# Kernel optimization log

Measured on AMD Instinct MI355X. Metric: run time of the kernel, lower is better.

The kernel has to match this reference:

```python
import jax, jax.numpy as jnp
import numpy as np
from jax import lax

B, D, H, W = 1, 16, 128, 128
CIN, NPTS = 16, 100000
NEG = np.float32(-1e30)  # stands in for -inf at unoccupied voxels in max pooling


def _conv(x, wk):
    # Minkowski stride-1 conv at occupied sites == dense zero-padded conv masked to occupancy
    return lax.conv_general_dilated(x, wk, (1, 1, 1), 'SAME',
                                    dimension_numbers=('NCDHW', 'OIDHW', 'NCDHW'))


def _crelu(x, wk, occ):
    return jnp.where(occ, jax.nn.relu(_conv(x, wk)), 0.0)


def _mpool(x, occ, spatial):
    # Minkowski max pool: max over occupied voxels in the kernel window; output coords are
    # the stride-floored input coords (z halved). spatial=True -> kernel (3,3,3) else (3,1,1).
    xm = jnp.where(occ, x, NEG)
    win = (1, 1, 3, 3, 3) if spatial else (1, 1, 3, 1, 1)
    pad = [(0, 0), (0, 0), (1, 1), (1, 1), (1, 1)] if spatial else [(0, 0), (0, 0), (1, 1), (0, 0), (0, 0)]
    y = lax.reduce_window(xm, NEG, lax.max, win, (1, 1, 2, 1, 1), pad)
    occ2 = occ[:, :, 0::2] | occ[:, :, 1::2]
    return jnp.where(occ2, y, 0.0), occ2


def _forward(voxel_features, coors, ws, batch_size):
    b, d, h, w = coors[:, 0], coors[:, 1], coors[:, 2], coors[:, 3]
    cin = voxel_features.shape[1]
    grid = jnp.zeros((batch_size, D, H, W, cin), voxel_features.dtype).at[b, d, h, w].set(voxel_features)
    x = jnp.transpose(grid, (0, 4, 1, 2, 3))  # (B, C, D, H, W)
    occ = jnp.zeros((batch_size, 1, D, H, W), bool).at[b, 0, d, h, w].set(True)

    x = _crelu(x, ws[0], occ)
    x = _crelu(x, ws[1], occ)
    x, occ = _mpool(x, occ, True)
    for wk in ws[2:5]:
        x = _crelu(x, wk, occ)
    x, occ = _mpool(x, occ, True)
    for wk in ws[5:8]:
        x = _crelu(x, wk, occ)
    x, occ = _mpool(x, occ, False)  # kernel (3,1,1)
    n, c, dd, hh, ww = x.shape  # (B, 64, 2, H, W)
    return x.reshape(n, c * dd, hh, ww)


def setup_inputs():
    key = jax.random.key(0)
    ks = jax.random.split(key, 9)
    rng = np.random.default_rng(0)
    lin = rng.permutation(D * H * W)[:NPTS].astype(np.int64)  # unique occupied voxels
    d = (lin // (H * W)).astype(np.int32)
    h = ((lin // W) % H).astype(np.int32)
    w = (lin % W).astype(np.int32)
    coors = jnp.asarray(np.stack([np.zeros(NPTS, np.int32), d, h, w], axis=1))
    vf = jax.random.normal(ks[0], (NPTS, CIN), jnp.float32)

    def cw(k, o, i):
        return jax.random.normal(k, (o, i, 3, 3, 3), jnp.float32) * np.float32(1.0 / np.sqrt(i * 27))

    chans = [(32, CIN), (64, 32)] + [(64, 64)] * 6
    ws = {f"w{j + 1}": cw(ks[j + 1], o, i) for j, (o, i) in enumerate(chans)}
    return dict(voxel_features=vf, coors=coors, batch_size=B, **ws)


def reference(voxel_features, coors, batch_size, w1, w2, w3, w4, w5, w6, w7, w8):
    return _forward(voxel_features, coors, (w1, w2, w3, w4, w5, w6, w7, w8), batch_size)
```

## Files before the change

### kernel.cpp

```cpp
#include <hip/hip_runtime.h>
#include <stdint.h>

#define DEV __device__ __forceinline__

typedef float f32x4 __attribute__((ext_vector_type(4)));
typedef short s16x8 __attribute__((ext_vector_type(8)));
typedef unsigned int u32x4 __attribute__((ext_vector_type(4)));
typedef unsigned int u32x2 __attribute__((ext_vector_type(2)));

static constexpr int HM = 128, WM = 128;
static constexpr int HP = 130, WP = 130;

DEV unsigned short f2bf(float f) {
  unsigned int u = __float_as_uint(f);
  return (unsigned short)((u + 0x7fffu + ((u >> 16) & 1u)) >> 16);
}
DEV float bf2f(unsigned short s) { return __uint_as_float(((unsigned int)s) << 16); }

DEV void gll16(const void* g, void* l) {
  __builtin_amdgcn_global_load_lds((const unsigned int*)g, (unsigned int*)l, 16, 0, 0);
}
DEV void waitvmc(int n) {
  if (n == 0)      asm volatile("s_waitcnt vmcnt(0)" ::: "memory");
  else if (n == 1) asm volatile("s_waitcnt vmcnt(1)" ::: "memory");
  else if (n == 2) asm volatile("s_waitcnt vmcnt(2)" ::: "memory");
  else if (n == 3) asm volatile("s_waitcnt vmcnt(3)" ::: "memory");
  else if (n == 4) asm volatile("s_waitcnt vmcnt(4)" ::: "memory");
  else if (n == 5) asm volatile("s_waitcnt vmcnt(5)" ::: "memory");
  else if (n == 7) asm volatile("s_waitcnt vmcnt(7)" ::: "memory");
  else             asm volatile("s_waitcnt vmcnt(0)" ::: "memory");
}

__global__ __launch_bounds__(256)
void scatter_k(const float* __restrict__ vf, const int* __restrict__ co,
               unsigned short* __restrict__ x,
               unsigned char* __restrict__ o0, unsigned char* __restrict__ o1,
               unsigned char* __restrict__ o2, unsigned char* __restrict__ o3,
               int npts) {
  int i = blockIdx.x * 256 + threadIdx.x;
  if (i >= npts) return;
  int d = co[i * 4 + 1], h = co[i * 4 + 2], w = co[i * 4 + 3];
  unsigned short* dst = x + (size_t)(((d + 1) * HP + (h + 1)) * WP + (w + 1)) * 32;
#pragma unroll
  for (int c = 0; c < 16; ++c) dst[c] = f2bf(vf[i * 16 + c]);
  int hw = h * WM + w;
  o0[d * (HM * WM) + hw] = 1;
  o1[(d >> 1) * (HM * WM) + hw] = 1;
  o2[(d >> 2) * (HM * WM) + hw] = 1;
  o3[(d >> 3) * (HM * WM) + hw] = 1;
}

__global__ __launch_bounds__(256)
void wcvt_all_k(const float* s0, const float* s1, const float* s2, const float* s3,
                const float* s4, const float* s5, const float* s6, const float* s7,
                unsigned short* __restrict__ dst) {
  int t = blockIdx.x * 256 + threadIdx.x;
  const int CIs[8] = {16, 32, 64, 64, 64, 64, 64, 64};
  const int CId[8] = {32, 32, 64, 64, 64, 64, 64, 64};
  const int COa[8] = {32, 64, 64, 64, 64, 64, 64, 64};
  const float* srcs[8] = {s0, s1, s2, s3, s4, s5, s6, s7};
  int start = 0;
#pragma unroll
  for (int i = 0; i < 8; ++i) {
    int sz = 27 * COa[i] * CId[i];
    if (t >= start && t < start + sz) {
      int l = t - start;
      int ci = l % CId[i];
      int r = l / CId[i];
      int cco = r % COa[i];
      int tap = r / COa[i];
      float v = (ci < CIs[i]) ? srcs[i][(cco * CIs[i] + ci) * 27 + tap] : 0.0f;
      dst[t] = f2bf(v);
    }
    start += sz;
  }
}

template <int CI, int CO, int ROWS>
__global__ __launch_bounds__(512, 4)
void conv_k(const unsigned short* __restrict__ xin, unsigned short* __restrict__ xout,
            const unsigned short* __restrict__ wt, const unsigned char* __restrict__ occ,
            int D) {
  constexpr int SLOTS = CI / 8;
  constexpr int MSK = SLOTS - 1;
  constexpr int CIB = CI / 32;
  constexpr int NM = CO / 16;
  constexpr int J = ROWS;
  constexpr int XROWS = ROWS + 2;
  constexpr int RXI = (128 * SLOTS) / 512;
  constexpr int NCW = 3 * CO * SLOTS;
  constexpr int KW = (NCW + 511) / 512;
  constexpr int NA = 2 * RXI + KW;
  constexpr int NB = RXI + KW;
  constexpr int WOFF = 3 * CO * CI;
  __shared__ __align__(16) unsigned short xs[XROWS * 130 * CI];
  __shared__ __align__(16) unsigned short wls[2 * WOFF];

  int nb = gridDim.x;
  int bid = blockIdx.x;
  int blk = (bid & 7) * (nb >> 3) + (bid >> 3);
  int tid = threadIdx.x;
  constexpr int HBLK = 128 / ROWS;
  int d = blk / HBLK, hb = blk - (blk / HBLK) * HBLK;
  int h0 = hb * ROWS;
  int lane = tid & 63, wv = tid >> 6, ln = lane & 15, lg = lane >> 4;

  auto issueX = [&](int kd, int ri) {
#pragma unroll
    for (int i = 0; i < RXI; ++i) {
      int c = i * 512 + tid;
      int vcol = 1 + c / SLOTS;
      int sl = c - (c / SLOTS) * SLOTS;
      int v = ri * 130 + vcol;
      int ss = sl ^ (v & MSK);
      const unsigned short* g =
          xin + ((size_t)((d + kd) * HP + (h0 + ri)) * WP + vcol) * CI + ss * 8;
      gll16(g, xs + (size_t)(ri * 130 + 1) * CI + (size_t)c * 8);
    }
  };
  auto issueW = [&](int kd, int kh, unsigned short* wbuf) {
#pragma unroll
    for (int i = 0; i < KW; ++i) {
      int c = i * 512 + tid;
      if (c >= NCW) c -= NCW;
      int u = c / SLOTS, sl = c - (c / SLOTS) * SLOTS;
      int kw = u / CO, cc = u - kw * CO;
      int ss = sl ^ (u & MSK);
      const unsigned short* g =
          wt + ((size_t)((kd * 3 + kh) * 3 + kw) * CO + cc) * CI + ss * 8;
      gll16(g, wbuf + (size_t)c * 8);
    }
  };

  {
    constexpr int CH8 = CO / 8;
    int hv = 2 * HP * WP + D * (2 * WP + 2 * HM);
    int tot8 = hv * CH8;
    int per = (tot8 + nb - 1) / nb;
    int base = blk * per, lim = base + per;
    if (lim > tot8) lim = tot8;
    for (int c = base + tid; c < lim; c += 512) {
      int i = c / CH8, sub = c - (c / CH8) * CH8;
      int p, hh, ww;
      if (i < 2 * HP * WP) {
        p = (i >= HP * WP) ? (D + 1) : 0;
        int rem = i - ((i >= HP * WP) ? HP * WP : 0);
        hh = rem / WP; ww = rem - hh * WP;
      } else {
        constexpr int PH = 2 * WP + 2 * HM;
        int j2 = i - 2 * HP * WP;
        p = j2 / PH + 1;
        int r2 = j2 - (p - 1) * PH;
        if (r2 < 2 * WP) { hh = (r2 >= WP) ? (HP - 1) : 0; ww = r2 % WP; }
        else { int r3 = r2 - 2 * WP; hh = 1 + (r3 & 127); ww = (r3 < HM) ? 0 : (WP - 1); }
      }
      *(u32x4*)(xout + ((size_t)(p * HP + hh) * WP + ww) * CO + sub * 8) = (u32x4)0u;
    }
  }
  issueX(0, 0);
  issueX(0, 1);
  issueW(0, 0, wls);
  for (int t = tid; t < XROWS * 2 * SLOTS; t += 512) {
    int ri = t / (2 * SLOTS);
    int r2 = t - ri * 2 * SLOTS;
    int colv = (r2 >= SLOTS) ? 129 : 0;
    int sl = r2 & MSK;
    *(u32x4*)(xs + (size_t)(ri * 130 + colv) * CI + sl * 8) = (u32x4)0u;
  }
  float on[J];
#pragma unroll
  for (int j = 0; j < J; ++j) {
    int vox = wv * (16 * J) + j * 16 + ln;
    on[j] = occ[(d * HM + (h0 + (vox >> 7))) * WM + (vox & 127)] ? 1.0f : 0.0f;
  }
  asm volatile("s_waitcnt lgkmcnt(0)" ::: "memory");

  f32x4 acc[NM][J];
#pragma unroll
  for (int m = 0; m < NM; ++m)
#pragma unroll
    for (int j = 0; j < J; ++j) acc[m][j] = (f32x4)0.0f;

#pragma unroll
  for (int s = 0; s < 9; ++s) {
    int kd = s / 3, kh = s - 3 * kd;
    unsigned short* wnext = wls + ((s + 1) & 1) * WOFF;
    if (kh == 0) {
#pragma unroll
      for (int ri = 2; ri < XROWS; ++ri) issueX(kd, ri);
      issueW(kd, 1, wnext);
    } else if (kh == 1) {
      if (kd < 2) issueX(kd + 1, 0);
      issueW(kd, 2, wnext);
    } else {
      if (kd < 2) {
        issueX(kd + 1, 1);
        issueW(kd + 1, 0, wnext);
      }
    }
    __builtin_amdgcn_sched_barrier(0);
    if (kh == 0)      waitvmc(NA);
    else if (kh == 1) waitvmc(kd < 2 ? NB : KW);
    else              waitvmc(kd < 2 ? NB : 0);
    __builtin_amdgcn_sched_barrier(0);
    __builtin_amdgcn_s_barrier();
    __builtin_amdgcn_sched_barrier(0);
    const unsigned short* wc = wls + (s & 1) * WOFF;
    __builtin_amdgcn_s_setprio(1);
#pragma unroll
    for (int kw = 0; kw < 3; ++kw) {
#pragma unroll
      for (int cb = 0; cb < CIB; ++cb) {
        int slot = cb * 4 + lg;
        s16x8 a[NM], b[J];
#pragma unroll
        for (int m = 0; m < NM; ++m) {
          int u = kw * CO + m * 16 + ln;
          a[m] = *(const s16x8*)(wc + ((size_t)u * SLOTS + (slot ^ (u & MSK))) * 8);
        }
#pragma unroll
        for (int j = 0; j < J; ++j) {
          int vox = wv * (16 * J) + j * 16 + ln;
          int v = ((vox >> 7) + kh) * 130 + (vox & 127) + kw;
          b[j] = *(const s16x8*)(xs + ((size_t)v * SLOTS + (slot ^ (v & MSK))) * 8);
        }
#pragma unroll
        for (int m = 0; m < NM; ++m)
#pragma unroll
          for (int j = 0; j < J; ++j)
            acc[m][j] = __builtin_amdgcn_mfma_f32_16x16x32_bf16(a[m], b[j], acc[m][j], 0, 0, 0);
      }
    }
    __builtin_amdgcn_s_setprio(0);
    __builtin_amdgcn_sched_barrier(0);
    if (s < 8) __builtin_amdgcn_s_barrier();
  }

#pragma unroll
  for (int j = 0; j < J; ++j) {
    int vox = wv * (16 * J) + j * 16 + ln;
    int r = vox >> 7, w2 = vox & 127;
    unsigned short* dst = xout + ((size_t)((d + 1) * HP + (h0 + r + 1)) * WP + (w2 + 1)) * CO;
#pragma unroll
    for (int m = 0; m < NM; ++m) {
      unsigned short q0 = f2bf(fmaxf(acc[m][j][0], 0.0f) * on[j]);
      unsigned short q1 = f2bf(fmaxf(acc[m][j][1], 0.0f) * on[j]);
      unsigned short q2 = f2bf(fmaxf(acc[m][j][2], 0.0f) * on[j]);
      unsigned short q3 = f2bf(fmaxf(acc[m][j][3], 0.0f) * on[j]);
      u32x2 pv;
      pv.x = (unsigned int)q0 | ((unsigned int)q1 << 16);
      pv.y = (unsigned int)q2 | ((unsigned int)q3 << 16);
      *(u32x2*)&dst[m * 16 + lg * 4] = pv;
    }
  }
}

template <int C>
__global__ __launch_bounds__(256)
void pool_sp_k(const unsigned short* __restrict__ xin, unsigned short* __restrict__ xout,
               const unsigned char* __restrict__ oc, int Dout) {
  constexpr int CH = C / 8;
  __shared__ __align__(16) unsigned short vm[WP * C];
  int row = blockIdx.x;
  int bh = row % HP, bdo = row / HP;
  int outRow = (bdo * HP + bh) * WP * C;
  int tid = threadIdx.x;
  if (bdo == 0 || bdo == Dout + 1 || bh == 0 || bh == HP - 1) {
    for (int i = tid; i < WP * C; i += 256) xout[outRow + i] = 0;
    return;
  }
  int dp = bdo - 1, h = bh - 1;

  for (int idx = tid; idx < WP * CH; idx += 256) {
    int w = idx / CH, c8 = idx - w * CH;
    float mx[8];
#pragma unroll
    for (int q = 0; q < 8; ++q) mx[q] = 0.0f;
#pragma unroll
    for (int dd = 0; dd < 3; ++dd)
#pragma unroll
      for (int hh = 0; hh < 3; ++hh) {
        const unsigned short* p =
            xin + ((size_t)((2 * dp + dd) * HP + (h + hh)) * WP + w) * C + c8 * 8;
        u32x4 v = *(const u32x4*)p;
        const unsigned short* u = (const unsigned short*)&v;
#pragma unroll
        for (int q = 0; q < 8; ++q) mx[q] = fmaxf(mx[q], bf2f(u[q]));
      }
    unsigned short o[8];
#pragma unroll
    for (int q = 0; q < 8; ++q) o[q] = f2bf(mx[q]);
    *(u32x4*)&vm[w * C + c8 * 8] = *(const u32x4*)o;
  }
  __syncthreads();

  for (int idx = tid; idx < WM * CH; idx += 256) {
    int w = idx / CH, c8 = idx - w * CH;
    float mx[8];
#pragma unroll
    for (int q = 0; q < 8; ++q) mx[q] = 0.0f;
#pragma unroll
    for (int ww = 0; ww < 3; ++ww) {
      u32x4 v = *(const u32x4*)&vm[(w + ww) * C + c8 * 8];
      const unsigned short* u = (const unsigned short*)&v;
#pragma unroll
      for (int q = 0; q < 8; ++q) mx[q] = fmaxf(mx[q], bf2f(u[q]));
    }
    bool on = oc[(dp * HM + h) * WM + w] != 0;
    unsigned short o[8];
#pragma unroll
    for (int q = 0; q < 8; ++q) o[q] = on ? f2bf(mx[q]) : (unsigned short)0;
    *(u32x4*)(xout + outRow + (w + 1) * C + c8 * 8) = *(const u32x4*)o;
  }
  for (int i = tid; i < 2 * C; i += 256) {
    int s = i / C, c = i - (i / C) * C;
    xout[outRow + (s ? (WP - 1) * C : 0) + c] = 0;
  }
}

__global__ __launch_bounds__(256)
void pool_d_k(const unsigned short* __restrict__ xin, float* __restrict__ out,
              const unsigned char* __restrict__ oc) {
  int t = blockIdx.x * 256 + threadIdx.x;
  int c8 = t & 7, w = (t >> 3) & 127, h = (t >> 10) & 127, dp = (t >> 17) & 1;
  float mx[8];
#pragma unroll
  for (int q = 0; q < 8; ++q) mx[q] = 0.0f;
#pragma unroll
  for (int dd = 0; dd < 3; ++dd) {
    const unsigned short* p =
        xin + ((size_t)((2 * dp + dd) * HP + (h + 1)) * WP + (w + 1)) * 64 + c8 * 8;
    u32x4 v = *(const u32x4*)p;
    const unsigned short* u = (const unsigned short*)&v;
#pragma unroll
    for (int q = 0; q < 8; ++q) mx[q] = fmaxf(mx[q], bf2f(u[q]));
  }
  bool on = oc[(dp * HM + h) * WM + w] != 0;
#pragma unroll
  for (int q = 0; q < 8; ++q) {
    int c = c8 * 8 + q;
    out[((c * 2 + dp) * HM + h) * WM + w] = on ? mx[q] : 0.0f;
  }
}

extern "C" void kernel_launch(void* const* d_in, const int* in_sizes, int n_in,
                              void* d_out, int out_size, void* d_ws, size_t ws_size,
                              hipStream_t stream) {
  (void)n_in; (void)out_size; (void)ws_size;
  const float* vf = (const float*)d_in[0];
  const int* co = (const int*)d_in[1];
  int npts = in_sizes[1] / 4;

  char* ws = (char*)d_ws;
  const size_t SA = (size_t)18 * 130 * 130 * 64 * 2;
  const size_t SB = (size_t)10 * 130 * 130 * 64 * 2;
  unsigned short* P = (unsigned short*)ws;
  unsigned short* Q = (unsigned short*)(ws + SA);
  unsigned short* R = P;
  unsigned char* occ0 = (unsigned char*)(ws + SA + SB);
  unsigned char* occ1 = occ0 + 16 * HM * WM;
  unsigned char* occ2 = occ1 + 8 * HM * WM;
  unsigned char* occ3 = occ2 + 4 * HM * WM;
  unsigned short* wb[8];
  {
    unsigned short* p = (unsigned short*)(occ3 + 2 * HM * WM);
    const int wsz[8] = {27 * 32 * 32, 27 * 64 * 32, 27 * 64 * 64, 27 * 64 * 64,
                        27 * 64 * 64, 27 * 64 * 64, 27 * 64 * 64, 27 * 64 * 64};
    for (int i = 0; i < 8; ++i) { wb[i] = p; p += wsz[i]; }
  }

  hipMemsetAsync(R, 0, (size_t)18 * 130 * 130 * 32 * 2, stream);
  hipMemsetAsync(occ0, 0, (size_t)(16 + 8 + 4 + 2) * HM * WM, stream);

  scatter_k<<<(npts + 255) / 256, 256, 0, stream>>>(vf, co, R, occ0, occ1, occ2, occ3, npts);

  {
    int tot = 27 * (32 * 32 + 64 * 32 + 6 * 64 * 64);
    wcvt_all_k<<<tot / 256, 256, 0, stream>>>(
        (const float*)d_in[3], (const float*)d_in[4], (const float*)d_in[5],
        (const float*)d_in[6], (const float*)d_in[7], (const float*)d_in[8],
        (const float*)d_in[9], (const float*)d_in[10], wb[0]);
  }

  conv_k<32, 32, 4><<<16 * 32, 512, 0, stream>>>(R, Q, wb[0], occ0, 16);
  conv_k<32, 64, 4><<<16 * 32, 512, 0, stream>>>(Q, P, wb[1], occ0, 16);
  pool_sp_k<64><<<10 * HP, 256, 0, stream>>>(P, Q, occ1, 8);
  conv_k<64, 64, 4><<<8 * 32, 512, 0, stream>>>(Q, P, wb[2], occ1, 8);
  conv_k<64, 64, 4><<<8 * 32, 512, 0, stream>>>(P, Q, wb[3], occ1, 8);
  conv_k<64, 64, 4><<<8 * 32, 512, 0, stream>>>(Q, P, wb[4], occ1, 8);
  pool_sp_k<64><<<6 * HP, 256, 0, stream>>>(P, Q, occ2, 4);
  conv_k<64, 64, 2><<<4 * 64, 512, 0, stream>>>(Q, P, wb[5], occ2, 4);
  conv_k<64, 64, 2><<<4 * 64, 512, 0, stream>>>(P, Q, wb[6], occ2, 4);
  conv_k<64, 64, 2><<<4 * 64, 512, 0, stream>>>(Q, P, wb[7], occ2, 4);
  pool_d_k<<<(2 * 128 * 128 * 8) / 256, 256, 0, stream>>>(P, (float*)d_out, occ3);
}
```

Measured before the change: 276.6 us.

## Tile spatial max-pool over four output rows with shared D-reduced halo

The spatial pooling kernel now processes four output H-rows per block. It first reduces over depth for six input rows and keeps them in shared memory, then does the 3x3 H/W max from LDS. Each D-reduced row is reused by three output rows instead of being reloaded from global memory. Halo zeroing is spread evenly across all blocks, and block IDs are swizzled. The grid shrinks from about 1300 blocks to 256/128, which cuts redundant global reads but lowers parallelism and uses more LDS per block.

```diff
diff --git a/kernel.cpp b/kernel.cpp
--- a/kernel.cpp
+++ b/kernel.cpp
@@ -260,61 +260,83 @@
 void pool_sp_k(const unsigned short* __restrict__ xin, unsigned short* __restrict__ xout,
                const unsigned char* __restrict__ oc, int Dout) {
   constexpr int CH = C / 8;
-  __shared__ __align__(16) unsigned short vm[WP * C];
-  int row = blockIdx.x;
-  int bh = row % HP, bdo = row / HP;
-  int outRow = (bdo * HP + bh) * WP * C;
+  __shared__ __align__(16) unsigned short dm[6 * WP * C];
+  int nb = gridDim.x;
+  int bid = blockIdx.x;
+  int blk = (bid & 7) * (nb >> 3) + (bid >> 3);
   int tid = threadIdx.x;
-  if (bdo == 0 || bdo == Dout + 1 || bh == 0 || bh == HP - 1) {
-    for (int i = tid; i < WP * C; i += 256) xout[outRow + i] = 0;
-    return;
-  }
-  int dp = bdo - 1, h = bh - 1;
-
-  for (int idx = tid; idx < WP * CH; idx += 256) {
-    int w = idx / CH, c8 = idx - w * CH;
+  int dp = blk >> 5, ht = blk & 31;
+  int h0 = ht * 4;
+
+  {
+    int hv = 2 * HP * WP + Dout * 2 * WP;
+    int tot8 = hv * CH;
+    int per = (tot8 + nb - 1) / nb;
+    int base = blk * per, lim = base + per;
+    if (lim > tot8) lim = tot8;
+    for (int c = base + tid; c < lim; c += 256) {
+      int i = c / CH, sub = c - (c / CH) * CH;
+      int p, hh, ww;
+      if (i < 2 * HP * WP) {
+        p = (i >= HP * WP) ? (Dout + 1) : 0;
+        int rem = i - ((i >= HP * WP) ? HP * WP : 0);
+        hh = rem / WP; ww = rem - hh * WP;
+      } else {
+        int j2 = i - 2 * HP * WP;
+        p = j2 / (2 * WP) + 1;
+        int r2 = j2 - (p - 1) * (2 * WP);
+        hh = (r2 >= WP) ? (HP - 1) : 0;
+        ww = r2 % WP;
+      }
+      *(u32x4*)(xout + ((size_t)(p * HP + hh) * WP + ww) * C + sub * 8) = (u32x4)0u;
+    }
+  }
+
+  for (int idx = tid; idx < 6 * WP * CH; idx += 256) {
+    int ri = idx / (WP * CH);
+    int rem = idx - ri * (WP * CH);
+    int w = rem / CH, c8 = rem - w * CH;
     float mx[8];
 #pragma unroll
     for (int q = 0; q < 8; ++q) mx[q] = 0.0f;
 #pragma unroll
-    for (int dd = 0; dd < 3; ++dd)
-#pragma unroll
-      for (int hh = 0; hh < 3; ++hh) {
-        const unsigned short* p =
-            xin + ((size_t)((2 * dp + dd) * HP + (h + hh)) * WP + w) * C + c8 * 8;
-        u32x4 v = *(const u32x4*)p;
+    for (int dd = 0; dd < 3; ++dd) {
+      const unsigned short* p =
+          xin + ((size_t)((2 * dp + dd) * HP + (h0 + ri)) * WP + w) * C + c8 * 8;
+      u32x4 v = *(const u32x4*)p;
+      const unsigned short* u = (const unsigned short*)&v;
+#pragma unroll
+      for (int q = 0; q < 8; ++q) mx[q] = fmaxf(mx[q], bf2f(u[q]));
+    }
+    unsigned short o[8];
+#pragma unroll
+    for (int q = 0; q < 8; ++q) o[q] = f2bf(mx[q]);
+    *(u32x4*)&dm[(size_t)(ri * WP + w) * C + c8 * 8] = *(const u32x4*)o;
+  }
+  __syncthreads();
+
+  for (int idx = tid; idx < 4 * WM * CH; idx += 256) {
+    int r = idx / (WM * CH);
+    int rem = idx - r * (WM * CH);
+    int w = rem / CH, c8 = rem - w * CH;
+    float mx[8];
+#pragma unroll
+    for (int q = 0; q < 8; ++q) mx[q] = 0.0f;
+#pragma unroll
+    for (int rr = 0; rr < 3; ++rr)
+#pragma unroll
+      for (int ww = 0; ww < 3; ++ww) {
+        u32x4 v = *(const u32x4*)&dm[(size_t)((r + rr) * WP + (w + ww)) * C + c8 * 8];
         const unsigned short* u = (const unsigned short*)&v;
 #pragma unroll
         for (int q = 0; q < 8; ++q) mx[q] = fmaxf(mx[q], bf2f(u[q]));
       }
+    bool onv = oc[(dp * HM + (h0 + r)) * WM + w] != 0;
     unsigned short o[8];
 #pragma unroll
-    for (int q = 0; q < 8; ++q) o[q] = f2bf(mx[q]);
-    *(u32x4*)&vm[w * C + c8 * 8] = *(const u32x4*)o;
-  }
-  __syncthreads();
-
-  for (int idx = tid; idx < WM * CH; idx += 256) {
-    int w = idx / CH, c8 = idx - w * CH;
-    float mx[8];
-#pragma unroll
-    for (int q = 0; q < 8; ++q) mx[q] = 0.0f;
-#pragma unroll
-    for (int ww = 0; ww < 3; ++ww) {
-      u32x4 v = *(const u32x4*)&vm[(w + ww) * C + c8 * 8];
-      const unsigned short* u = (const unsigned short*)&v;
-#pragma unroll
-      for (int q = 0; q < 8; ++q) mx[q] = fmaxf(mx[q], bf2f(u[q]));
-    }
-    bool on = oc[(dp * HM + h) * WM + w] != 0;
-    unsigned short o[8];
-#pragma unroll
-    for (int q = 0; q < 8; ++q) o[q] = on ? f2bf(mx[q]) : (unsigned short)0;
-    *(u32x4*)(xout + outRow + (w + 1) * C + c8 * 8) = *(const u32x4*)o;
-  }
-  for (int i = tid; i < 2 * C; i += 256) {
-    int s = i / C, c = i - (i / C) * C;
-    xout[outRow + (s ? (WP - 1) * C : 0) + c] = 0;
+    for (int q = 0; q < 8; ++q) o[q] = onv ? f2bf(mx[q]) : (unsigned short)0;
+    *(u32x4*)(xout + ((size_t)((dp + 1) * HP + (h0 + r + 1)) * WP + (w + 1)) * C + c8 * 8) =
+        *(const u32x4*)o;
   }
 }
 
@@ -384,11 +406,11 @@
 
   conv_k<32, 32, 4><<<16 * 32, 512, 0, stream>>>(R, Q, wb[0], occ0, 16);
   conv_k<32, 64, 4><<<16 * 32, 512, 0, stream>>>(Q, P, wb[1], occ0, 16);
-  pool_sp_k<64><<<10 * HP, 256, 0, stream>>>(P, Q, occ1, 8);
+  pool_sp_k<64><<<8 * 32, 256, 0, stream>>>(P, Q, occ1, 8);
   conv_k<64, 64, 4><<<8 * 32, 512, 0, stream>>>(Q, P, wb[2], occ1, 8);
   conv_k<64, 64, 4><<<8 * 32, 512, 0, stream>>>(P, Q, wb[3], occ1, 8);
   conv_k<64, 64, 4><<<8 * 32, 512, 0, stream>>>(Q, P, wb[4], occ1, 8);
-  pool_sp_k<64><<<6 * HP, 256, 0, stream>>>(P, Q, occ2, 4);
+  pool_sp_k<64><<<4 * 32, 256, 0, stream>>>(P, Q, occ2, 4);
   conv_k<64, 64, 2><<<4 * 64, 512, 0, stream>>>(Q, P, wb[5], occ2, 4);
   conv_k<64, 64, 2><<<4 * 64, 512, 0, stream>>>(P, Q, wb[6], occ2, 4);
   conv_k<64, 64, 2><<<4 * 64, 512, 0, stream>>>(Q, P, wb[7], occ2, 4);
```

Result: slower. 282.6 us (+2.2%).
